# Kernel optimization log

Measured on AMD Instinct MI355X. Metric: run time of the kernel, lower is better.

## Reference

```python
import jax, jax.numpy as jnp
import numpy as np

B, S, DIM, H = 2, 2048, 1024, 16
HD = DIM // H  # 64


def setup_inputs() -> dict:
    key = jax.random.key(0)
    ks = jax.random.split(key, 7)
    sc = 1.0 / np.sqrt(DIM)
    gammas = jnp.asarray(1.0 - 2.0 ** (-5.0 - np.arange(H)), jnp.float32)  # RetNet per-head decay
    return {
        "q": jax.random.normal(ks[0], (B, S, DIM), jnp.float32),
        "k": jax.random.normal(ks[1], (B, S, DIM), jnp.float32),
        "v": jax.random.normal(ks[2], (B, S, DIM), jnp.float32),
        "W_in": jax.random.normal(ks[3], (DIM, DIM), jnp.float32) * sc,
        "b_in": jnp.zeros((DIM,), jnp.float32),
        "W_gate": jax.random.normal(ks[4], (DIM, DIM), jnp.float32) * sc,
        "b_gate": jnp.zeros((DIM,), jnp.float32),
        "W_out": jax.random.normal(ks[5], (DIM, DIM), jnp.float32) * sc,
        "b_out": jnp.zeros((DIM,), jnp.float32),
        "gammas": gammas,
    }


def _mamba(x, W_in, b_in, W_gate, b_gate, W_out, b_out):
    # Gated linear recurrence: h_t = a_t * h_{t-1} + u_t  (selective-scan style)
    u = x @ W_in + b_in          # [B,S,D]
    a = jax.nn.sigmoid(x @ W_gate + b_gate)  # [B,S,D] data-dependent decay gate

    def combine(c1, c2):
        a1, u1 = c1
        a2, u2 = c2
        return (a1 * a2, a2 * u1 + u2)

    _, h = jax.lax.associative_scan(combine, (a, u), axis=1)  # parallel scan over S
    return h @ W_out + b_out  # residual=False, dropout=0.0


def _retention(q, k, v, gammas):
    # Per-head decay-masked attention: out = ((Q K^T / sqrt(hd)) * D) V,
    # D[h,n,m] = gamma_h^(n-m) for n>=m else 0 (causal decay kernel).
    def split(x):
        return x.reshape(B, S, H, HD).transpose(0, 2, 1, 3)  # [B,H,S,HD]

    qh, kh, vh = split(q), split(k), split(v)
    idx = jnp.arange(S)
    diff = idx[:, None] - idx[None, :]                        # [S,S]
    expnt = jnp.maximum(diff, 0).astype(jnp.float32)
    D = jnp.where(diff >= 0, gammas[:, None, None] ** expnt, 0.0)  # [H,S,S]
    scores = jnp.einsum("bhnd,bhmd->bhnm", qh, kh) / np.sqrt(HD)
    out = jnp.einsum("bhnm,bhmd->bhnd", scores * D[None], vh)
    return out.transpose(0, 2, 1, 3).reshape(B, S, DIM)


def reference(q, k, v, W_in, b_in, W_gate, b_gate, W_out, b_out, gammas):
    q_proj = _mamba(q, W_in, b_in, W_gate, b_gate, W_out, b_out)
    return _retention(q_proj, k, v, gammas)
```

## Files before the change

### kernel.cpp

```cpp
#include <hip/hip_runtime.h>
#include <math.h>

#define B_  2
#define S_  2048
#define D_  1024
#define H_  16
#define HD_ 64
#define M_  (B_*S_)

typedef unsigned short ushort_t;
typedef unsigned int   uint_t;
typedef __attribute__((ext_vector_type(8))) short bf16x8;
typedef __attribute__((ext_vector_type(4))) float f32x4;

__device__ __forceinline__ ushort_t f2bf(float f) {
    uint_t u = __builtin_bit_cast(uint_t, f);
    u += 0x7FFFu + ((u >> 16) & 1u);
    return (ushort_t)(u >> 16);
}
__device__ __forceinline__ float bf2f(ushort_t h) {
    uint_t u = (uint_t)h << 16;
    return __builtin_bit_cast(float, u);
}
__device__ __forceinline__ uint_t pkt(float lo, float hi) {
    return __builtin_amdgcn_perm(__builtin_bit_cast(uint_t, hi),
                                 __builtin_bit_cast(uint_t, lo), 0x07060302u);
}
__device__ __forceinline__ void dma16(const ushort_t* g, ushort_t* l) {
    __builtin_amdgcn_global_load_lds(
        (const __attribute__((address_space(1))) uint_t*)g,
        (__attribute__((address_space(3))) uint_t*)l, 16, 0, 0);
}
__device__ __forceinline__ bf16x8 fragr(const ushort_t* base, int row, int chunk) {
    return *(const bf16x8*)&base[row * 64 + (((chunk ^ (row & 7)) << 3))];
}

__global__ __launch_bounds__(256)
void prep(const float* __restrict__ W0, const float* __restrict__ W1,
          const float* __restrict__ W2, ushort_t* __restrict__ T0,
          ushort_t* __restrict__ T1, ushort_t* __restrict__ T2,
          const float* __restrict__ X, ushort_t* __restrict__ Y) {
    const int bx = blockIdx.x;
    if (bx >= 3072) {
        const int i = ((bx - 3072) * 256 + threadIdx.x) * 4;
        float4 x = *(const float4*)(X + i);
        *(ushort4*)(Y + i) = make_ushort4(f2bf(x.x), f2bf(x.y), f2bf(x.z), f2bf(x.w));
        return;
    }
    __shared__ float T[32][36];
    const int z = bx >> 10;
    const float*  W  = (z == 0) ? W0 : (z == 1) ? W1 : W2;
    ushort_t*     WT = (z == 0) ? T0 : (z == 1) ? T1 : T2;
    const int kt = bx & 31, nt = (bx >> 5) & 31;
    const int t = threadIdx.x;
    const int rr = t >> 3, cc = (t & 7) * 4;
    float4 w4 = *(const float4*)(W + (size_t)(kt * 32 + rr) * D_ + nt * 32 + cc);
    T[rr][cc + 0] = w4.x; T[rr][cc + 1] = w4.y; T[rr][cc + 2] = w4.z; T[rr][cc + 3] = w4.w;
    __syncthreads();
    ushort_t o[4];
    #pragma unroll
    for (int j = 0; j < 4; ++j) o[j] = f2bf(T[cc + j][rr]);
    *(ushort4*)(WT + (size_t)(nt * 32 + rr) * D_ + kt * 32 + cc) =
        make_ushort4(o[0], o[1], o[2], o[3]);
}

__global__ __launch_bounds__(256)
void gemm_dual_kv(const ushort_t* __restrict__ A, const ushort_t* __restrict__ BTi,
                  const ushort_t* __restrict__ BTg, const float* __restrict__ bi,
                  const float* __restrict__ bg, float* __restrict__ Hloc,
                  ushort_t* __restrict__ Pp, float* __restrict__ cA,
                  float* __restrict__ cU,
                  const float* __restrict__ K, const float* __restrict__ V,
                  const float* __restrict__ gammas, ushort_t* __restrict__ Kb,
                  ushort_t* __restrict__ VT, float* __restrict__ Gg) {
    __shared__ ushort_t smem[32768];
    const int tid = threadIdx.x;
    const int w = tid >> 6, lane = tid & 63, quad = lane >> 4, l15 = lane & 15;

    if (blockIdx.x >= 512) {
        ushort_t* Tv = smem;
        ushort_t* Tk = smem + 64 * 72;
        const int idx = blockIdx.x - 512;
        const int mt = idx & 31, h = (idx >> 5) & 15, b = idx >> 9;
        const int m0 = mt * 64;
        const int r = tid >> 2, c0 = (tid & 3) * 16;
        const float lg = log2f(gammas[h]);
        const float gm = exp2f(-(float)r * lg);
        {
            const float* src = K + ((size_t)(b * S_ + m0 + r)) * D_ + h * HD_ + c0;
            ushort_t kb[16];
            #pragma unroll
            for (int j4 = 0; j4 < 4; ++j4) {
                float4 x = *(const float4*)(src + j4 * 4);
                kb[j4 * 4 + 0] = f2bf(x.x); kb[j4 * 4 + 1] = f2bf(x.y);
                kb[j4 * 4 + 2] = f2bf(x.z); kb[j4 * 4 + 3] = f2bf(x.w);
            }
            ushort_t* dst = Kb + ((size_t)(b * S_ + m0 + r)) * D_ + h * HD_ + c0;
            *(uint4*)(dst + 0) = *(const uint4*)&kb[0];
            *(uint4*)(dst + 8) = *(const uint4*)&kb[8];
            #pragma unroll
            for (int j = 0; j < 16; ++j) Tk[(c0 + j) * 72 + r] = kb[j];
        }
        {
            const float* src = V + ((size_t)(b * S_ + m0 + r)) * D_ + h * HD_ + c0;
            #pragma unroll
            for (int j4 = 0; j4 < 4; ++j4) {
                float4 x = *(const float4*)(src + j4 * 4);
                Tv[(c0 + j4 * 4 + 0) * 72 + r] = f2bf(x.x * gm);
                Tv[(c0 + j4 * 4 + 1) * 72 + r] = f2bf(x.y * gm);
                Tv[(c0 + j4 * 4 + 2) * 72 + r] = f2bf(x.z * gm);
                Tv[(c0 + j4 * 4 + 3) * 72 + r] = f2bf(x.w * gm);
            }
        }
        __syncthreads();
        {
            ushort_t* dst = VT + ((size_t)((b * H_ + h) * HD_ + r)) * S_ + m0 + c0;
            *(uint4*)(dst + 0) = *(const uint4*)&Tv[r * 72 + c0 + 0];
            *(uint4*)(dst + 8) = *(const uint4*)&Tv[r * 72 + c0 + 8];
        }
        bf16x8 af0 = *(const bf16x8*)&Tv[(w * 16 + l15) * 72 + quad * 8];
        bf16x8 af1 = *(const bf16x8*)&Tv[(w * 16 + l15) * 72 + 32 + quad * 8];
        float* gout = Gg + ((size_t)((b * H_ + h) * 32 + mt)) * 4096;
        #pragma unroll
        for (int kt2 = 0; kt2 < 4; ++kt2) {
            bf16x8 bf0 = *(const bf16x8*)&Tk[(kt2 * 16 + l15) * 72 + quad * 8];
            bf16x8 bf1 = *(const bf16x8*)&Tk[(kt2 * 16 + l15) * 72 + 32 + quad * 8];
            f32x4 g = {};
            g = __builtin_amdgcn_mfma_f32_16x16x32_bf16(af0, bf0, g, 0, 0, 0);
            g = __builtin_amdgcn_mfma_f32_16x16x32_bf16(af1, bf1, g, 0, 0, 0);
            #pragma unroll
            for (int reg = 0; reg < 4; ++reg)
                gout[(w * 16 + quad * 4 + reg) * 64 + kt2 * 16 + l15] = g[reg];
        }
        return;
    }

    const int n0 = (blockIdx.x & 15) * 64, m0 = (blockIdx.x >> 4) * 128;
    const int wr = (w >> 1) * 64, wc = (w & 1) * 32;
    const int l8 = lane & 7, lr8 = lane >> 3;

    f32x4 acc_i[4][2] = {};
    f32x4 acc_g[4][2] = {};

    auto stage = [&](int k0, int bufo) {
        #pragma unroll
        for (int t = 0; t < 4; ++t) {
            const int row = w * 32 + t * 8 + lr8;
            const int gc = ((l8 ^ (row & 7)) << 3);
            dma16(A + (size_t)(m0 + row) * D_ + k0 + gc, &smem[bufo + row * 64 + l8 * 8]);
        }
        #pragma unroll
        for (int t = 0; t < 2; ++t) {
            const int row = w * 16 + t * 8 + lr8;
            const int gc = ((l8 ^ (row & 7)) << 3);
            dma16(BTi + (size_t)(n0 + row) * D_ + k0 + gc, &smem[bufo + 8192 + row * 64 + l8 * 8]);
            dma16(BTg + (size_t)(n0 + row) * D_ + k0 + gc, &smem[bufo + 12288 + row * 64 + l8 * 8]);
        }
    };

    stage(0, 0);
    __syncthreads();
    for (int t = 0; t < 16; ++t) {
        const int bufo = (t & 1) * 16384;
        if (t < 15) stage((t + 1) * 64, 16384 - bufo);
        const ushort_t* As = smem + bufo;
        const ushort_t* Bi = smem + bufo + 8192;
        const ushort_t* Bg = smem + bufo + 12288;
        #pragma unroll
        for (int kk = 0; kk < 2; ++kk) {
            bf16x8 af[4], bfi[2], bfg[2];
            #pragma unroll
            for (int i = 0; i < 4; ++i)
                af[i] = fragr(As, wr + 16 * i + l15, kk * 4 + quad);
            #pragma unroll
            for (int j = 0; j < 2; ++j) {
                bfi[j] = fragr(Bi, wc + 16 * j + l15, kk * 4 + quad);
                bfg[j] = fragr(Bg, wc + 16 * j + l15, kk * 4 + quad);
            }
            #pragma unroll
            for (int i = 0; i < 4; ++i)
                #pragma unroll
                for (int j = 0; j < 2; ++j) {
                    acc_i[i][j] = __builtin_amdgcn_mfma_f32_16x16x32_bf16(
                        af[i], bfi[j], acc_i[i][j], 0, 0, 0);
                    acc_g[i][j] = __builtin_amdgcn_mfma_f32_16x16x32_bf16(
                        af[i], bfg[j], acc_g[i][j], 0, 0, 0);
                }
        }
        __syncthreads();
    }

    ushort_t* Us = smem;
    ushort_t* Gu = smem + 8448;
    #pragma unroll
    for (int j = 0; j < 2; ++j) {
        const int n = wc + 16 * j + l15;
        const float bbi = bi[n0 + n], bbg = bg[n0 + n];
        #pragma unroll
        for (int i = 0; i < 4; ++i) {
            #pragma unroll
            for (int r = 0; r < 4; ++r) {
                const int m = wr + 16 * i + quad * 4 + r;
                Us[m * 66 + n] = f2bf(acc_i[i][j][r] + bbi);
                float g = 1.0f / (1.0f + __expf(-(acc_g[i][j][r] + bbg)));
                Gu[m * 66 + n] = (ushort_t)__float2uint_rn(g * 65535.0f);
            }
        }
    }
    __syncthreads();

    const int nl = tid & 63, c = tid >> 6;
    const int gmb = m0 + c * 32;
    const size_t gbase = (size_t)gmb * D_ + n0 + nl;
    float Aa = 1.0f, hh = 0.0f;
    #pragma unroll 4
    for (int j = 0; j < 32; ++j) {
        const float g = (float)Gu[(c * 32 + j) * 66 + nl] * (1.0f / 65535.0f);
        const float u = bf2f(Us[(c * 32 + j) * 66 + nl]);
        Aa *= g;
        hh = fmaf(g, hh, u);
        Pp[gbase + (size_t)j * D_] = f2bf(Aa);
        Hloc[gbase + (size_t)j * D_] = hh;
    }
    const int bb = gmb >> 11;
    const int ch = (gmb & 2047) >> 5;
    const int ci = ((bb * 64 + ch) << 10) + n0 + nl;
    cA[ci] = Aa;
    cU[ci] = hh;
}

__global__ __launch_bounds__(256)
void mid_scan(const float* __restrict__ Gg, const float* __restrict__ gammas,
              ushort_t* __restrict__ Sb, const float* __restrict__ cA,
              const float* __restrict__ cU, float* __restrict__ cIn) {
    const int bi = blockIdx.x;
    if (bi < 128) {
        const int sl = bi & 3, h = (bi >> 2) & 15, b = bi >> 6;
        const float g64 = exp2f(64.0f * log2f(gammas[h]));
        const int r = threadIdx.x >> 4;
        const int cb = (threadIdx.x & 15) * 4;
        const size_t base = ((size_t)((b * H_ + h) * 32)) * 4096 + (sl * 16 + r) * 64 + cb;
        float4 S = make_float4(0.f, 0.f, 0.f, 0.f);
        for (int c = 0; c < 32; ++c) {
            ushort4 sb;
            sb.x = f2bf(S.x); sb.y = f2bf(S.y); sb.z = f2bf(S.z); sb.w = f2bf(S.w);
            *(ushort4*)(Sb + base + (size_t)c * 4096) = sb;
            float4 G = *(const float4*)(Gg + base + (size_t)c * 4096);
            S.x = g64 * (S.x + G.x); S.y = g64 * (S.y + G.y);
            S.z = g64 * (S.z + G.z); S.w = g64 * (S.w + G.w);
        }
        return;
    }
    const int t = (bi - 128) * 256 + threadIdx.x;
    const int d = t & 1023, b = t >> 10;
    float h = 0.0f;
    for (int c0 = 0; c0 < 64; c0 += 16) {
        float Av[16], Uv[16];
        #pragma unroll
        for (int j = 0; j < 16; ++j) {
            const int idx = ((b * 64 + c0 + j) << 10) + d;
            Av[j] = cA[idx]; Uv[j] = cU[idx];
        }
        #pragma unroll
        for (int j = 0; j < 16; ++j) {
            cIn[((b * 64 + c0 + j) << 10) + d] = h;
            h = fmaf(Av[j], h, Uv[j]);
        }
    }
}

__global__ __launch_bounds__(256)
void scan_fix(const float* __restrict__ Hloc, const ushort_t* __restrict__ Pp,
              const float* __restrict__ cIn, ushort_t* __restrict__ hout) {
    const int i = (blockIdx.x * 256 + threadIdx.x) * 4;
    const int m = i >> 10, d = i & 1023;
    const int b = m >> 11, ch = (m & 2047) >> 5;
    float4 hl = *(const float4*)(Hloc + i);
    ushort4 p4 = *(const ushort4*)(Pp + i);
    float4 ci = *(const float4*)(cIn + ((b * 64 + ch) << 10) + d);
    ushort4 o;
    o.x = f2bf(fmaf(ci.x, bf2f(p4.x), hl.x));
    o.y = f2bf(fmaf(ci.y, bf2f(p4.y), hl.y));
    o.z = f2bf(fmaf(ci.z, bf2f(p4.z), hl.z));
    o.w = f2bf(fmaf(ci.w, bf2f(p4.w), hl.w));
    *(ushort4*)(hout + i) = o;
}

__global__ __launch_bounds__(256)
void gemm_out_ret(const ushort_t* __restrict__ A, const ushort_t* __restrict__ BT,
                  const float* __restrict__ bias, const ushort_t* __restrict__ Kb,
                  const ushort_t* __restrict__ VT, const ushort_t* __restrict__ Sb,
                  const float* __restrict__ gammas, float* __restrict__ Out) {
    __shared__ ushort_t smem[24576];
    const int tid = threadIdx.x;
    const int h = blockIdx.x;
    const int n0 = h * 64, m0 = blockIdx.y * 128;
    const int w = tid >> 6, lane = tid & 63, quad = lane >> 4, l15 = lane & 15;
    const int wr = (w >> 1) * 64, wc = (w & 1) * 32;
    const int l8 = lane & 7, lr8 = lane >> 3;

    f32x4 acc[4][2] = {};

    auto stage = [&](int k0, int bufo) {
        #pragma unroll
        for (int t = 0; t < 4; ++t) {
            const int row = w * 32 + t * 8 + lr8;
            const int gc = ((l8 ^ (row & 7)) << 3);
            dma16(A + (size_t)(m0 + row) * D_ + k0 + gc, &smem[bufo + row * 64 + l8 * 8]);
        }
        #pragma unroll
        for (int t = 0; t < 2; ++t) {
            const int row = w * 16 + t * 8 + lr8;
            const int gc = ((l8 ^ (row & 7)) << 3);
            dma16(BT + (size_t)(n0 + row) * D_ + k0 + gc, &smem[bufo + 8192 + row * 64 + l8 * 8]);
        }
    };

    stage(0, 0);
    __syncthreads();
    for (int t = 0; t < 16; ++t) {
        const int bufo = (t & 1) * 12288;
        if (t < 15) stage((t + 1) * 64, 12288 - bufo);
        const ushort_t* As = smem + bufo;
        const ushort_t* Bs = smem + bufo + 8192;
        #pragma unroll
        for (int kk = 0; kk < 2; ++kk) {
            bf16x8 af[4], bf[2];
            #pragma unroll
            for (int i = 0; i < 4; ++i)
                af[i] = fragr(As, wr + 16 * i + l15, kk * 4 + quad);
            #pragma unroll
            for (int j = 0; j < 2; ++j)
                bf[j] = fragr(Bs, wc + 16 * j + l15, kk * 4 + quad);
            #pragma unroll
            for (int i = 0; i < 4; ++i)
                #pragma unroll
                for (int j = 0; j < 2; ++j)
                    acc[i][j] = __builtin_amdgcn_mfma_f32_16x16x32_bf16(
                        af[i], bf[j], acc[i][j], 0, 0, 0);
        }
        __syncthreads();
    }

    ushort_t* Qs = smem;
    ushort_t* Ks = smem + 8192;
    ushort_t* Vt = smem + 12288;
    ushort_t* Ss = smem + 16384;
    ushort_t* Ps = smem + 20480;
    #pragma unroll
    for (int j = 0; j < 2; ++j) {
        const int n = wc + 16 * j + l15;
        const float bb = bias[n0 + n];
        #pragma unroll
        for (int i = 0; i < 4; ++i)
            #pragma unroll
            for (int r = 0; r < 4; ++r) {
                const int m = wr + 16 * i + quad * 4 + r;
                Qs[m * 64 + (((n >> 3) ^ (m & 7)) << 3) + (n & 7)] =
                    f2bf((acc[i][j][r] + bb) * 0.125f);
            }
    }
    __syncthreads();

    const float lg = log2f(gammas[h]);
    const int nl = w * 16 + l15;

    for (int sc = 0; sc < 2; ++sc) {
        const int mrow = m0 + sc * 64;
        const int bb2 = mrow >> 11;
        const int s0 = mrow & 2047;
        const int nt2 = s0 >> 6;
        const size_t bS = (size_t)bb2 * S_;
        const size_t vrow0 = (size_t)((bb2 * H_ + h) * HD_);
        const size_t sbase = ((size_t)((bb2 * H_ + h) * 32 + nt2)) * 4096;
        const ushort_t* Qsub = Qs + sc * 64 * 64;

        #pragma unroll
        for (int t = 0; t < 2; ++t) {
            const int row = w * 16 + t * 8 + lr8;
            const int gc = ((l8 ^ (row & 7)) << 3);
            dma16(Kb + (bS + s0 + row) * D_ + h * HD_ + gc, &Ks[row * 64 + l8 * 8]);
            dma16(VT + (vrow0 + row) * S_ + s0 + gc, &Vt[row * 64 + l8 * 8]);
            dma16(Sb + sbase + (size_t)row * 64 + gc, &Ss[row * 64 + l8 * 8]);
        }
        __syncthreads();

        bf16x8 qf0 = fragr(Qsub, nl, quad);
        bf16x8 qf1 = fragr(Qsub, nl, 4 + quad);

        f32x4 o[4] = {};
        #pragma unroll
        for (int ct = 0; ct < 4; ++ct) {
            bf16x8 sf0 = fragr(Ss, ct * 16 + l15, quad);
            bf16x8 sf1 = fragr(Ss, ct * 16 + l15, 4 + quad);
            o[ct] = __builtin_amdgcn_mfma_f32_16x16x32_bf16(sf0, qf0, o[ct], 0, 0, 0);
            o[ct] = __builtin_amdgcn_mfma_f32_16x16x32_bf16(sf1, qf1, o[ct], 0, 0, 0);
        }
        #pragma unroll
        for (int mt2 = 0; mt2 < 4; ++mt2) {
            bf16x8 kf0 = fragr(Ks, mt2 * 16 + l15, quad);
            bf16x8 kf1 = fragr(Ks, mt2 * 16 + l15, 4 + quad);
            f32x4 s = {};
            s = __builtin_amdgcn_mfma_f32_16x16x32_bf16(kf0, qf0, s, 0, 0, 0);
            s = __builtin_amdgcn_mfma_f32_16x16x32_bf16(kf1, qf1, s, 0, 0, 0);
            const int mbase = mt2 * 16 + quad * 4;
            #pragma unroll
            for (int r = 0; r < 4; ++r)
                if (nl < mbase + r) s[r] = 0.0f;
            uint2 pw; pw.x = pkt(s[0], s[1]); pw.y = pkt(s[2], s[3]);
            const int chunk = mbase >> 3;
            *(uint2*)&Ps[nl * 64 + ((chunk ^ (nl & 7)) << 3) + (mbase & 7)] = pw;
        }
        bf16x8 pf0 = fragr(Ps, nl, quad);
        bf16x8 pf1 = fragr(Ps, nl, 4 + quad);
        #pragma unroll
        for (int ct = 0; ct < 4; ++ct) {
            bf16x8 vf0 = fragr(Vt, ct * 16 + l15, quad);
            bf16x8 vf1 = fragr(Vt, ct * 16 + l15, 4 + quad);
            o[ct] = __builtin_amdgcn_mfma_f32_16x16x32_bf16(vf0, pf0, o[ct], 0, 0, 0);
            o[ct] = __builtin_amdgcn_mfma_f32_16x16x32_bf16(vf1, pf1, o[ct], 0, 0, 0);
        }

        const float esc = exp2f((float)nl * lg);
        const size_t ob = (bS + s0 + nl) * D_ + h * HD_;
        #pragma unroll
        for (int ct = 0; ct < 4; ++ct) {
            f32x4 t = o[ct] * esc;
            *(f32x4*)(Out + ob + ct * 16 + quad * 4) = t;
        }
        __syncthreads();
    }
}

extern "C" void kernel_launch(void* const* d_in, const int* in_sizes, int n_in,
                              void* d_out, int out_size, void* d_ws, size_t ws_size,
                              hipStream_t stream) {
    const float* q      = (const float*)d_in[0];
    const float* k      = (const float*)d_in[1];
    const float* v      = (const float*)d_in[2];
    const float* W_in   = (const float*)d_in[3];
    const float* b_in   = (const float*)d_in[4];
    const float* W_gate = (const float*)d_in[5];
    const float* b_gate = (const float*)d_in[6];
    const float* W_out  = (const float*)d_in[7];
    const float* b_out  = (const float*)d_in[8];
    const float* gammas = (const float*)d_in[9];
    float* out = (float*)d_out;

    char* ws = (char*)d_ws;
    const size_t MB = 1024 * 1024;
    float*    Hloc    = (float*)(ws);
    ushort_t* Pp      = (ushort_t*)(ws + 16 * MB);
    ushort_t* h_bf    = (ushort_t*)(ws + 24 * MB);
    ushort_t* q_bf    = (ushort_t*)(ws + 32 * MB);
    ushort_t* WT_in   = (ushort_t*)(ws + 40 * MB);
    ushort_t* WT_gate = (ushort_t*)(ws + 42 * MB);
    ushort_t* WT_out  = (ushort_t*)(ws + 44 * MB);
    float*    cA      = (float*)(ws + 46 * MB);
    float*    cU      = (float*)(ws + 46 * MB + 512 * 1024);
    float*    cIn     = (float*)(ws + 47 * MB);
    ushort_t* k_bf    = (ushort_t*)(ws + 48 * MB);
    ushort_t* VT      = (ushort_t*)(ws + 56 * MB);
    float*    Gg      = (float*)(ws + 64 * MB);
    ushort_t* Sb      = (ushort_t*)(ws + 80 * MB);

    prep<<<3072 + (M_ * D_) / (256 * 4), 256, 0, stream>>>(
        W_in, W_gate, W_out, WT_in, WT_gate, WT_out, q, q_bf);

    gemm_dual_kv<<<512 + 1024, 256, 0, stream>>>(
        q_bf, WT_in, WT_gate, b_in, b_gate, Hloc, Pp, cA, cU,
        k, v, gammas, k_bf, VT, Gg);

    mid_scan<<<136, 256, 0, stream>>>(Gg, gammas, Sb, cA, cU, cIn);
    scan_fix<<<(M_ * D_) / 1024, 256, 0, stream>>>(Hloc, Pp, cIn, h_bf);

    gemm_out_ret<<<dim3(H_, M_ / 128), 256, 0, stream>>>(
        h_bf, WT_out, b_out, k_bf, VT, Sb, gammas, out);
}
```

Before: 178.6 us.

## Prefetch retention K/V/S tiles during GEMM tail and swizzle block order

In the fused output-GEMM plus retention kernel, the K, V and S tile loads are issued early so they overlap with compute. K is loaded during the last GEMM iteration, V and S during the Q epilogue, and next-chunk tiles during the current chunk's compute. The P writes are deferred behind a barrier so the buffers can be reused safely. Both GEMM kernels also remap their block index with a swizzle, so that blocks running at the same time share A or B tiles in L2. The cost is extra barriers, a few more live registers, and more complex buffer-reuse ordering.

```diff
diff --git a/kernel.cpp b/kernel.cpp
--- a/kernel.cpp
+++ b/kernel.cpp
@@ -135,7 +135,8 @@
         return;
     }
 
-    const int n0 = (blockIdx.x & 15) * 64, m0 = (blockIdx.x >> 4) * 128;
+    const int swz = (blockIdx.x & 7) * 64 + (blockIdx.x >> 3);
+    const int n0 = (swz & 15) * 64, m0 = (swz >> 4) * 128;
     const int wr = (w >> 1) * 64, wc = (w & 1) * 32;
     const int l8 = lane & 7, lr8 = lane >> 3;
 
@@ -293,11 +294,52 @@
                   const float* __restrict__ gammas, float* __restrict__ Out) {
     __shared__ ushort_t smem[24576];
     const int tid = threadIdx.x;
-    const int h = blockIdx.x;
-    const int n0 = h * 64, m0 = blockIdx.y * 128;
+    const int flat = blockIdx.x + (blockIdx.y << 4);
+    const int swz = (flat & 7) * 64 + (flat >> 3);
+    const int h = swz & 15;
+    const int n0 = h * 64, m0 = (swz >> 4) * 128;
     const int w = tid >> 6, lane = tid & 63, quad = lane >> 4, l15 = lane & 15;
     const int wr = (w >> 1) * 64, wc = (w & 1) * 32;
     const int l8 = lane & 7, lr8 = lane >> 3;
+
+    ushort_t* Qs = smem;
+    ushort_t* Ks = smem + 8192;
+    ushort_t* Vt = smem + 12288;
+    ushort_t* Ss = smem + 16384;
+    ushort_t* Ps = smem + 20480;
+
+    auto stageK = [&](int sc) {
+        const int mrow = m0 + sc * 64;
+        const size_t bS2 = (size_t)(mrow >> 11) * S_;
+        const int s0r = mrow & 2047;
+        #pragma unroll
+        for (int t2 = 0; t2 < 2; ++t2) {
+            const int row = w * 16 + t2 * 8 + lr8;
+            const int gc = ((l8 ^ (row & 7)) << 3);
+            dma16(Kb + (bS2 + s0r + row) * D_ + h * HD_ + gc, &Ks[row * 64 + l8 * 8]);
+        }
+    };
+    auto stageV = [&](int sc) {
+        const int mrow = m0 + sc * 64;
+        const size_t vrow0 = (size_t)(((mrow >> 11) * H_ + h) * HD_);
+        const int s0r = mrow & 2047;
+        #pragma unroll
+        for (int t2 = 0; t2 < 2; ++t2) {
+            const int row = w * 16 + t2 * 8 + lr8;
+            const int gc = ((l8 ^ (row & 7)) << 3);
+            dma16(VT + (vrow0 + row) * S_ + s0r + gc, &Vt[row * 64 + l8 * 8]);
+        }
+    };
+    auto stageS = [&](int sc) {
+        const int mrow = m0 + sc * 64;
+        const size_t sbase = ((size_t)(((mrow >> 11) * H_ + h) * 32 + ((mrow & 2047) >> 6))) * 4096;
+        #pragma unroll
+        for (int t2 = 0; t2 < 2; ++t2) {
+            const int row = w * 16 + t2 * 8 + lr8;
+            const int gc = ((l8 ^ (row & 7)) << 3);
+            dma16(Sb + sbase + (size_t)row * 64 + gc, &Ss[row * 64 + l8 * 8]);
+        }
+    };
 
     f32x4 acc[4][2] = {};
 
@@ -321,6 +363,7 @@
     for (int t = 0; t < 16; ++t) {
         const int bufo = (t & 1) * 12288;
         if (t < 15) stage((t + 1) * 64, 12288 - bufo);
+        if (t == 15) stageK(0);
         const ushort_t* As = smem + bufo;
         const ushort_t* Bs = smem + bufo + 8192;
         #pragma unroll
@@ -342,11 +385,9 @@
         __syncthreads();
     }
 
-    ushort_t* Qs = smem;
-    ushort_t* Ks = smem + 8192;
-    ushort_t* Vt = smem + 12288;
-    ushort_t* Ss = smem + 16384;
-    ushort_t* Ps = smem + 20480;
+    stageV(0);
+    stageS(0);
+
     #pragma unroll
     for (int j = 0; j < 2; ++j) {
         const int n = wc + 16 * j + l15;
@@ -360,30 +401,16 @@
                     f2bf((acc[i][j][r] + bb) * 0.125f);
             }
     }
-    __syncthreads();
 
     const float lg = log2f(gammas[h]);
     const int nl = w * 16 + l15;
 
     for (int sc = 0; sc < 2; ++sc) {
+        __syncthreads();
         const int mrow = m0 + sc * 64;
-        const int bb2 = mrow >> 11;
+        const size_t bS = (size_t)(mrow >> 11) * S_;
         const int s0 = mrow & 2047;
-        const int nt2 = s0 >> 6;
-        const size_t bS = (size_t)bb2 * S_;
-        const size_t vrow0 = (size_t)((bb2 * H_ + h) * HD_);
-        const size_t sbase = ((size_t)((bb2 * H_ + h) * 32 + nt2)) * 4096;
         const ushort_t* Qsub = Qs + sc * 64 * 64;
-
-        #pragma unroll
-        for (int t = 0; t < 2; ++t) {
-            const int row = w * 16 + t * 8 + lr8;
-            const int gc = ((l8 ^ (row & 7)) << 3);
-            dma16(Kb + (bS + s0 + row) * D_ + h * HD_ + gc, &Ks[row * 64 + l8 * 8]);
-            dma16(VT + (vrow0 + row) * S_ + s0 + gc, &Vt[row * 64 + l8 * 8]);
-            dma16(Sb + sbase + (size_t)row * 64 + gc, &Ss[row * 64 + l8 * 8]);
-        }
-        __syncthreads();
 
         bf16x8 qf0 = fragr(Qsub, nl, quad);
         bf16x8 qf1 = fragr(Qsub, nl, 4 + quad);
@@ -396,6 +423,7 @@
             o[ct] = __builtin_amdgcn_mfma_f32_16x16x32_bf16(sf0, qf0, o[ct], 0, 0, 0);
             o[ct] = __builtin_amdgcn_mfma_f32_16x16x32_bf16(sf1, qf1, o[ct], 0, 0, 0);
         }
+        uint2 pw[4];
         #pragma unroll
         for (int mt2 = 0; mt2 < 4; ++mt2) {
             bf16x8 kf0 = fragr(Ks, mt2 * 16 + l15, quad);
@@ -407,9 +435,15 @@
             #pragma unroll
             for (int r = 0; r < 4; ++r)
                 if (nl < mbase + r) s[r] = 0.0f;
-            uint2 pw; pw.x = pkt(s[0], s[1]); pw.y = pkt(s[2], s[3]);
+            pw[mt2].x = pkt(s[0], s[1]); pw[mt2].y = pkt(s[2], s[3]);
+        }
+        __syncthreads();
+        if (sc == 0) { stageK(1); stageS(1); }
+        #pragma unroll
+        for (int mt2 = 0; mt2 < 4; ++mt2) {
+            const int mbase = mt2 * 16 + quad * 4;
             const int chunk = mbase >> 3;
-            *(uint2*)&Ps[nl * 64 + ((chunk ^ (nl & 7)) << 3) + (mbase & 7)] = pw;
+            *(uint2*)&Ps[nl * 64 + ((chunk ^ (nl & 7)) << 3) + (mbase & 7)] = pw[mt2];
         }
         bf16x8 pf0 = fragr(Ps, nl, quad);
         bf16x8 pf1 = fragr(Ps, nl, 4 + quad);
@@ -429,6 +463,7 @@
             *(f32x4*)(Out + ob + ct * 16 + quad * 4) = t;
         }
         __syncthreads();
+        if (sc == 0) stageV(1);
     }
 }
 
```

After: 174.5 us. -2.3%, faster.
